# Kernel optimization log

Hardware: AMD Instinct MI355X
Metric: run time of the kernel (lower is better)

Reference implementation:

```python
import jax, jax.numpy as jnp
from jax import lax
import numpy as np

THRESHOLD = 0.9
KHALF = 5  # conv_kernel_size; full conv width = 2*KHALF + 1 = 11


def _cif_scan(eouts, alpha_norm, elens, ylens, Lp1):
    """Vectorized-over-batch integrate-and-fire scan over time (lax.scan)."""
    B, T, D = eouts.shape
    bidx = jnp.arange(B)
    dt = eouts.dtype

    def step(carry, xs):
        alpha_accum, state, n_tok, fired = carry
        a_t, e_t, t = xs  # a_t: [B], e_t: [B,D], t: scalar int
        alpha_accum = alpha_accum + a_t
        active = (t <= elens - 1) & (n_tok < ylens)
        fire = active & (alpha_accum >= THRESHOLD)
        ak1 = 1.0 - alpha_accum
        ak2 = a_t - ak1
        # attention-weight column for time t
        aw_col = jnp.zeros((B, Lp1), dt)
        w_old = jnp.where(fire, ak1, jnp.where(active, a_t, jnp.zeros((), dt)))
        aw_col = aw_col.at[bidx, n_tok].add(w_old)
        n_new = n_tok + fire.astype(n_tok.dtype)
        aw_col = aw_col.at[bidx, n_new].add(jnp.where(fire, ak2, jnp.zeros((), dt)))
        # fired output row (set once per token slot)
        fire_val = state + ak1[:, None] * e_t
        cur = fired[bidx, n_tok]
        fired = fired.at[bidx, n_tok].set(jnp.where(fire[:, None], fire_val, cur))
        # integrate / reset state
        state = jnp.where(fire[:, None], ak2[:, None] * e_t,
                          jnp.where(active[:, None], state + a_t[:, None] * e_t, state))
        alpha_accum = jnp.where(fire, ak2, alpha_accum)
        return (alpha_accum, state, n_new, fired), aw_col

    init = (jnp.zeros((B,), dt), jnp.zeros((B, D), dt),
            jnp.zeros((B,), jnp.int32), jnp.zeros((B, Lp1, D), dt))
    xs = (jnp.swapaxes(alpha_norm, 0, 1), jnp.swapaxes(eouts, 0, 1),
          jnp.arange(T))
    (_, _, _, fired), aw_cols = lax.scan(step, init, xs)
    aws = jnp.transpose(aw_cols, (1, 2, 0))[:, None]  # [B,1,Lp1,T]
    return fired, aws


def _forward(eouts, conv_w, conv_b, proj_w, proj_b, elens, ylens, L):
    # Conv1d over time, 'same' padding: [B,T,D] -> [B,T,C]
    conv_feat = lax.conv_general_dilated(
        eouts, conv_w, window_strides=(1,), padding=[(KHALF, KHALF)],
        dimension_numbers=('NWC', 'WIO', 'NWC')) + conv_b
    alpha = jax.nn.sigmoid(conv_feat @ proj_w + proj_b)[:, :, 0]  # [B,T]
    alpha_norm = alpha / jnp.sum(alpha, axis=1, keepdims=True) \
        * ylens[:, None].astype(alpha.dtype)
    fired, aws = _cif_scan(eouts, alpha_norm, elens, ylens, L + 1)
    return fired[:, :L], alpha, aws


def setup_inputs():
    key = jax.random.key(0)
    k1, k2, k3, k4, k5 = jax.random.split(key, 5)
    B, T, D, C = 16, 2048, 512, 512
    eouts = jax.random.normal(k1, (B, T, D), jnp.float32)
    elens = jnp.maximum(jax.random.randint(k2, (B,), 0, T), T // 2).astype(jnp.int32)
    ylens = jnp.maximum(jax.random.randint(k3, (B,), 0, 128), 32).astype(jnp.int32)
    conv_w = jax.random.normal(k4, (2 * KHALF + 1, D, C), jnp.float32) * 0.02
    conv_b = jnp.zeros((C,), jnp.float32)
    proj_w = jax.random.normal(k5, (C, 1), jnp.float32) * 0.05
    proj_b = jnp.zeros((1,), jnp.float32)
    return dict(eouts=eouts, conv_w=conv_w, conv_b=conv_b,
                proj_w=proj_w, proj_b=proj_b, elens=elens, ylens=ylens)


def reference(eouts, conv_w, conv_b, proj_w, proj_b, elens, ylens):
    L = int(jnp.max(ylens))  # max_len = ylens.max(), as in the original
    return _forward(eouts, conv_w, conv_b, proj_w, proj_b, elens, ylens, L)
```

## Files before the change

kernel.cpp:

```cpp
#include <hip/hip_runtime.h>
#include <math.h>

#define KHALF 5
#define MAXF 256

__device__ inline float readlane_f(float v, int lane) {
    return __int_as_float(__builtin_amdgcn_readlane(__float_as_int(v), lane));
}

__global__ void k_prep(const float* __restrict__ conv_w, const float* __restrict__ conv_b,
                       const float* __restrict__ proj_w, const float* __restrict__ proj_b,
                       float* __restrict__ w_eff, float* __restrict__ b_eff,
                       int KD, int C,
                       float* __restrict__ aws, long long awsN, int WB, int NFILL) {
    if ((int)blockIdx.x >= WB) {
        long long N4 = awsN >> 2;
        long long gid = (long long)(blockIdx.x - WB) * 256 + threadIdx.x;
        float4 z = make_float4(0.f, 0.f, 0.f, 0.f);
        float4* a4 = reinterpret_cast<float4*>(aws);
        long long stride = (long long)NFILL * 256;
        for (long long i = gid; i < N4; i += stride) a4[i] = z;
        int tail = (int)(awsN & 3);
        if (gid < tail) aws[4 * N4 + gid] = 0.f;
        return;
    }
    int gid = blockIdx.x * blockDim.x + threadIdx.x;
    int wave = gid >> 6;
    int lane = gid & 63;
    if (wave > KD) return;
    float s = 0.f;
    if (wave < KD) {
        const float* row = conv_w + (size_t)wave * C;
        for (int c = lane * 4; c < C; c += 256) {
            float4 v = *reinterpret_cast<const float4*>(row + c);
            float4 w = *reinterpret_cast<const float4*>(proj_w + c);
            s += v.x * w.x + v.y * w.y + v.z * w.z + v.w * w.w;
        }
    } else {
        for (int c = lane; c < C; c += 64) s += conv_b[c] * proj_w[c];
    }
#pragma unroll
    for (int off = 32; off > 0; off >>= 1) s += __shfl_down(s, off, 64);
    if (lane == 0) {
        if (wave < KD) w_eff[wave] = s;
        else           b_eff[0] = s + proj_b[0];
    }
}

__global__ __launch_bounds__(256) void k_qdot(const float* __restrict__ eouts,
                                              const float* __restrict__ w_eff,
                                              float* __restrict__ q, int BT) {
    __shared__ float tile[64 * 68];
    __shared__ float wls[11 * 68];
    __shared__ float part[64 * 89];
    const int u0 = blockIdx.x * 64;
    const int rp = threadIdx.x & 31;
    const int s8 = threadIdx.x >> 5;
    float acc0[11], acc1[11];
#pragma unroll
    for (int k = 0; k < 11; ++k) { acc0[k] = 0.f; acc1[k] = 0.f; }
    for (int c = 0; c < 8; ++c) {
        __syncthreads();
#pragma unroll
        for (int it = 0; it < 4; ++it) {
            int idx = it * 256 + threadIdx.x;
            int r = idx >> 4, j4 = idx & 15;
            float4 v = *reinterpret_cast<const float4*>(
                eouts + (size_t)(u0 + r) * 512 + c * 64 + j4 * 4);
            *reinterpret_cast<float4*>(&tile[r * 68 + j4 * 4]) = v;
        }
        if (threadIdx.x < 176) {
            int k = threadIdx.x >> 4, sl = threadIdx.x & 15;
            float4 wv = *reinterpret_cast<const float4*>(
                w_eff + k * 512 + c * 64 + sl * 4);
            *reinterpret_cast<float4*>(&wls[k * 68 + sl * 4]) = wv;
        }
        __syncthreads();
#pragma unroll
        for (int j4 = 0; j4 < 2; ++j4) {
            const int dl = s8 * 8 + j4 * 4;
            float4 a0 = *reinterpret_cast<const float4*>(&tile[rp * 68 + dl]);
            float4 a1 = *reinterpret_cast<const float4*>(&tile[(rp + 32) * 68 + dl]);
#pragma unroll
            for (int k = 0; k < 11; ++k) {
                float4 wv = *reinterpret_cast<const float4*>(&wls[k * 68 + dl]);
                acc0[k] += a0.x * wv.x + a0.y * wv.y + a0.z * wv.z + a0.w * wv.w;
                acc1[k] += a1.x * wv.x + a1.y * wv.y + a1.z * wv.z + a1.w * wv.w;
            }
        }
    }
    __syncthreads();
#pragma unroll
    for (int k = 0; k < 11; ++k) {
        part[rp * 89 + s8 * 11 + k] = acc0[k];
        part[(rp + 32) * 89 + s8 * 11 + k] = acc1[k];
    }
    __syncthreads();
    if (threadIdx.x < 64) {
        int r = threadIdx.x;
        const float* p = &part[r * 89];
        float o[12];
#pragma unroll
        for (int k = 0; k < 11; ++k) {
            float s0 = (p[0 * 11 + k] + p[1 * 11 + k]) + (p[2 * 11 + k] + p[3 * 11 + k]);
            float s1 = (p[4 * 11 + k] + p[5 * 11 + k]) + (p[6 * 11 + k] + p[7 * 11 + k]);
            o[k] = s0 + s1;
        }
        o[11] = 0.f;
        float4* dst = reinterpret_cast<float4*>(q + (size_t)(u0 + r) * 12);
        dst[0] = make_float4(o[0], o[1], o[2], o[3]);
        dst[1] = make_float4(o[4], o[5], o[6], o[7]);
        dst[2] = make_float4(o[8], o[9], o[10], o[11]);
    }
}

__global__ __launch_bounds__(256) void k_sigpart(const float* __restrict__ q,
                                                 const float* __restrict__ b_eff,
                                                 float* __restrict__ alpha,
                                                 float* __restrict__ partials,
                                                 int T, int tcb) {
    __shared__ float qs[266 * 12];
    __shared__ float psm[4];
    int bx = blockIdx.x;
    int b = bx / tcb, tc = bx % tcb;
    int t0 = tc * 256;
    const float* qb = q + (size_t)b * T * 12;
    const int base = (t0 - 5) * 12;
    const int lim = T * 12;
    for (int i = threadIdx.x; i < 266 * 12; i += 256) {
        int gi = base + i;
        qs[i] = (gi >= 0 && gi < lim) ? qb[gi] : 0.f;
    }
    __syncthreads();
    int t = t0 + threadIdx.x;
    float sacc = b_eff[0];
#pragma unroll
    for (int k = 0; k < 11; ++k) sacc += qs[(threadIdx.x + k) * 12 + k];
    float al = 1.f / (1.f + expf(-sacc));
    alpha[(size_t)b * T + t] = al;
    float s = al;
    int lane = threadIdx.x & 63;
    int w = threadIdx.x >> 6;
#pragma unroll
    for (int off = 32; off > 0; off >>= 1) s += __shfl_down(s, off, 64);
    if (lane == 0) psm[w] = s;
    __syncthreads();
    if (threadIdx.x == 0) {
        float tot = 0.f;
        for (int i = 0; i < 4; ++i) tot += psm[i];
        partials[bx] = tot;
    }
}

__global__ void k_alpha(const float* __restrict__ eouts,
                        const float* __restrict__ w_eff,
                        const float* __restrict__ b_eff,
                        float* __restrict__ alpha,
                        int B, int T, int D) {
    const int W = 2 * KHALF + 1;
    int gid = blockIdx.x * blockDim.x + threadIdx.x;
    int wave = gid >> 6;
    int lane = gid & 63;
    if (wave >= B * T) return;
    int b = wave / T;
    int t = wave - b * T;
    int WD = W * D;
    int t0 = t - KHALF;
    float s = 0.f;
    if (t0 >= 0 && t0 + W <= T) {
        const float* base = eouts + ((size_t)b * T + t0) * D;
        for (int j = lane * 4; j < WD; j += 256) {
            float4 v = *reinterpret_cast<const float4*>(base + j);
            float4 w = *reinterpret_cast<const float4*>(w_eff + j);
            s += v.x * w.x + v.y * w.y + v.z * w.z + v.w * w.w;
        }
    } else {
        const float* base = eouts + (size_t)b * T * D;
        for (int j = lane; j < WD; j += 64) {
            int tt = t0 + j / D;
            if (tt >= 0 && tt < T) {
                int d = j - (j / D) * D;
                s += base[(size_t)tt * D + d] * w_eff[j];
            }
        }
    }
#pragma unroll
    for (int off = 32; off > 0; off >>= 1) s += __shfl_down(s, off, 64);
    if (lane == 0) {
        float logit = s + b_eff[0];
        alpha[(size_t)b * T + t] = 1.f / (1.f + expf(-logit));
    }
}

__global__ void k_chain(const float* __restrict__ alpha_in,
                        int use_part,
                        const float* __restrict__ partials, int npart,
                        const int* __restrict__ elens,
                        const int* __restrict__ ylens,
                        float* __restrict__ anorm,
                        int* __restrict__ n_fired,
                        int* __restrict__ fire_t,
                        float* __restrict__ fire_a1,
                        float* __restrict__ fire_a2,
                        int T, int Lp1) {
    extern __shared__ float an[];
    float* pf = an + T;
    __shared__ float sm[16];
    __shared__ float stot;
    int b = blockIdx.x;
    const float* row = alpha_in + (size_t)b * T;
    if ((T & 1023) == 0) {
        const float4* r4 = reinterpret_cast<const float4*>(row);
        float4* a4 = reinterpret_cast<float4*>(an);
        for (int i = threadIdx.x; i < (T >> 2); i += blockDim.x) a4[i] = r4[i];
    } else {
        for (int i = threadIdx.x; i < T; i += blockDim.x) an[i] = row[i];
    }
    __syncthreads();
    if (use_part) {
        if (threadIdx.x < npart && threadIdx.x < 16)
            sm[threadIdx.x] = partials[b * npart + threadIdx.x];
        __syncthreads();
        if (threadIdx.x == 0) {
            float tot = 0.f;
            if (npart <= 16) { for (int i = 0; i < npart; ++i) tot += sm[i]; }
            else { for (int i = 0; i < npart; ++i) tot += partials[b * npart + i]; }
            stot = tot;
        }
    } else {
        float s = 0.f;
        for (int i = threadIdx.x; i < T; i += blockDim.x) s += an[i];
        int lane0 = threadIdx.x & 63;
        int w0 = threadIdx.x >> 6;
#pragma unroll
        for (int off = 32; off > 0; off >>= 1) s += __shfl_down(s, off, 64);
        if (lane0 == 0) sm[w0] = s;
        __syncthreads();
        if (threadIdx.x == 0) {
            float tot = 0.f;
            int nw = blockDim.x >> 6;
            for (int i = 0; i < nw; ++i) tot += sm[i];
            stot = tot;
        }
    }
    __syncthreads();
    float ssum = stot;
    float yl = (float)ylens[b];
    float* __restrict__ anb = anorm + (size_t)b * T;
    for (int i = threadIdx.x; i < T; i += blockDim.x) {
        float v = an[i] / ssum * yl;
        an[i] = v;
        anb[i] = v;
    }
    __syncthreads();
    {
        int wv = threadIdx.x >> 6, ln = threadIdx.x & 63;
        int nchunks = (T + 63) >> 6;
        for (int c = wv; c < nchunks; c += 4) {
            int t = c * 64 + ln;
            float P = (t < T) ? an[t] : 0.f;
#pragma unroll
            for (int off = 1; off < 64; off <<= 1) {
                float tmp = __shfl_up(P, off, 64);
                if (ln >= off) P += tmp;
            }
            if (t < T) pf[t] = P;
        }
    }
    __syncthreads();
    if (threadIdx.x >= 64) return;
    int lane = threadIdx.x;
    int elen = elens[b];
    if (elen > T) elen = T;
    const int ylen = ylens[b];
    int* __restrict__ ft = fire_t + (size_t)b * Lp1;
    float* __restrict__ fa1 = fire_a1 + (size_t)b * Lp1;
    float* __restrict__ fa2 = fire_a2 + (size_t)b * Lp1;
    float accum = 0.f;
    int n = 0;
    bool done = false;
    for (int t0 = 0; t0 < elen && !done; t0 += 64) {
        int nv = elen - t0;
        if (nv > 64) nv = 64;
        bool inb = (t0 + lane < T);
        float P = inb ? pf[t0 + lane] : 0.f;
        float av = inb ? an[t0 + lane] : 0.f;
        unsigned long long validmask = (nv == 64) ? ~0ull : ((1ull << nv) - 1ull);
        float base = accum;
        int start = 0;
        while (true) {
            bool cond = (base + P >= 0.9f);
            unsigned long long bal = __ballot(cond) & validmask;
            if (start > 0) bal &= (~0ull) << start;
            if (bal == 0) break;
            int u = __builtin_ctzll(bal);
            float Pu = readlane_f(P, u);
            float au = readlane_f(av, u);
            float accum_f = base + Pu;
            float ak1 = 1.f - accum_f;
            float ak2 = au - ak1;
            if (lane == 0) { ft[n] = t0 + u; fa1[n] = ak1; fa2[n] = ak2; }
            ++n;
            if (n >= ylen) { done = true; break; }
            base = ak2 - Pu;
            start = u + 1;
            if (start >= nv) break;
        }
        if (!done) accum = base + readlane_f(P, nv - 1);
    }
    if (lane == 0) n_fired[b] = n;
}

__global__ void k_awfired(const float* __restrict__ eouts,
                          const float* __restrict__ anorm,
                          const int* __restrict__ elens,
                          const int* __restrict__ ylens,
                          const int* __restrict__ n_fired,
                          const int* __restrict__ fire_t,
                          const float* __restrict__ fire_a1,
                          const float* __restrict__ fire_a2,
                          float* __restrict__ aws,
                          float* __restrict__ fired,
                          int T, int D, int L, int Lp1,
                          int AB, int tcpb) {
    if ((int)blockIdx.x < AB) {
        __shared__ int fts[MAXF];
        __shared__ float a1s[MAXF];
        __shared__ float a2s[MAXF];
        int b = blockIdx.x / tcpb;
        int tc = blockIdx.x % tcpb;
        int nf = n_fired[b];
        for (int i = threadIdx.x; i < nf; i += blockDim.x) {
            fts[i] = fire_t[(size_t)b * Lp1 + i];
            a1s[i] = fire_a1[(size_t)b * Lp1 + i];
            a2s[i] = fire_a2[(size_t)b * Lp1 + i];
        }
        __syncthreads();
        int t = tc * 256 + threadIdx.x;
        if (t >= T) return;
        int elen = elens[b];
        if (elen > T) elen = T;
        int ylen = ylens[b];
        if (t >= elen) return;
        int lo = 0, hi = nf;
        while (lo < hi) {
            int mid = (lo + hi) >> 1;
            if (fts[mid] < t) lo = mid + 1; else hi = mid;
        }
        int rowi = lo;
        bool isfire = (rowi < nf && fts[rowi] == t);
        float* col = aws + (size_t)b * Lp1 * T + t;
        if (isfire) {
            col[(size_t)rowi * T] = a1s[rowi];
            col[(size_t)(rowi + 1) * T] = a2s[rowi];
        } else if (rowi < ylen) {
            col[(size_t)rowi * T] = anorm[(size_t)b * T + t];
        }
    } else {
        __shared__ float4 red[128];
        int idx = blockIdx.x - AB;
        int b = idx / L;
        int n = idx % L;
        int h = threadIdx.x >> 7;
        int dl = threadIdx.x & 127;
        int nf = n_fired[b];
        if ((D & 3) == 0) {
            int D4 = D >> 2;
            float4* dst = reinterpret_cast<float4*>(fired + ((size_t)b * L + n) * D);
            if (n >= nf) {
                if (h == 0) {
                    for (int d4 = dl; d4 < D4; d4 += 128)
                        dst[d4] = make_float4(0.f, 0.f, 0.f, 0.f);
                }
                return;
            }
            int t0 = (n == 0) ? 0 : fire_t[(size_t)b * Lp1 + n - 1];
            int t1 = fire_t[(size_t)b * Lp1 + n];
            float ak1 = fire_a1[(size_t)b * Lp1 + n];
            float ak2p = (n > 0) ? fire_a2[(size_t)b * Lp1 + n - 1] : 0.f;
            const float* an_g = anorm + (size_t)b * T;
            float wfirst = (n > 0) ? ak2p : an_g[t0];
            int len = t1 - t0 + 1;
            int half0 = len >> 1;
            int ts = h ? (t0 + half0) : t0;
            int te = h ? t1 : (t0 + half0 - 1);
            const float4* Eb = reinterpret_cast<const float4*>(eouts + (size_t)b * T * D);
            for (int d0 = 0; d0 < D4; d0 += 128) {
                int d4 = d0 + dl;
                float4 acc = make_float4(0.f, 0.f, 0.f, 0.f);
                if (d4 < D4 && ts <= te) {
                    float4 a0 = acc, a1 = acc, a2 = acc, a3 = acc;
                    int t = ts;
                    const float4* ee = Eb + (size_t)ts * D4 + d4;
                    for (; t + 3 <= te; t += 4, ee += 4 * (size_t)D4) {
                        float w0 = (t == t1)     ? ak1 : ((t == t0)     ? wfirst : an_g[t]);
                        float w1 = (t + 1 == t1) ? ak1 : an_g[t + 1];
                        float w2 = (t + 2 == t1) ? ak1 : an_g[t + 2];
                        float w3 = (t + 3 == t1) ? ak1 : an_g[t + 3];
                        float4 va = ee[0], vb = ee[D4], vc = ee[2 * (size_t)D4], vd = ee[3 * (size_t)D4];
                        a0.x += w0 * va.x; a0.y += w0 * va.y; a0.z += w0 * va.z; a0.w += w0 * va.w;
                        a1.x += w1 * vb.x; a1.y += w1 * vb.y; a1.z += w1 * vb.z; a1.w += w1 * vb.w;
                        a2.x += w2 * vc.x; a2.y += w2 * vc.y; a2.z += w2 * vc.z; a2.w += w2 * vc.w;
                        a3.x += w3 * vd.x; a3.y += w3 * vd.y; a3.z += w3 * vd.z; a3.w += w3 * vd.w;
                    }
                    for (; t <= te; ++t, ee += D4) {
                        float wt = (t == t1) ? ak1 : ((t == t0) ? wfirst : an_g[t]);
                        float4 v = ee[0];
                        a0.x += wt * v.x; a0.y += wt * v.y; a0.z += wt * v.z; a0.w += wt * v.w;
                    }
                    acc.x = (a0.x + a1.x) + (a2.x + a3.x);
                    acc.y = (a0.y + a1.y) + (a2.y + a3.y);
                    acc.z = (a0.z + a1.z) + (a2.z + a3.z);
                    acc.w = (a0.w + a1.w) + (a2.w + a3.w);
                }
                if (h == 1 && d4 < D4) red[dl] = acc;
                __syncthreads();
                if (h == 0 && d4 < D4) {
                    float4 o = red[dl];
                    acc.x += o.x; acc.y += o.y; acc.z += o.z; acc.w += o.w;
                    dst[d4] = acc;
                }
                __syncthreads();
            }
        } else {
            float* dst = fired + ((size_t)b * L + n) * D;
            if (n >= nf) {
                for (int d = threadIdx.x; d < D; d += 256) dst[d] = 0.f;
                return;
            }
            int t0 = (n == 0) ? 0 : fire_t[(size_t)b * Lp1 + n - 1];
            int t1 = fire_t[(size_t)b * Lp1 + n];
            float ak1 = fire_a1[(size_t)b * Lp1 + n];
            float ak2p = (n > 0) ? fire_a2[(size_t)b * Lp1 + n - 1] : 0.f;
            const float* an_g = anorm + (size_t)b * T;
            for (int d = threadIdx.x; d < D; d += 256) {
                const float* e = eouts + ((size_t)b * T + t0) * D + d;
                float accv;
                if (t1 == t0) {
                    accv = ak1 * e[0];
                } else {
                    float w0 = (n > 0) ? ak2p : an_g[t0];
                    accv = w0 * e[0];
                    float a0 = 0.f, a1 = 0.f, a2 = 0.f, a3 = 0.f;
                    int t = t0 + 1;
                    const float* ee = e + D;
                    for (; t + 3 < t1; t += 4, ee += 4 * (size_t)D) {
                        a0 += an_g[t]     * ee[0];
                        a1 += an_g[t + 1] * ee[D];
                        a2 += an_g[t + 2] * ee[2 * (size_t)D];
                        a3 += an_g[t + 3] * ee[3 * (size_t)D];
                    }
                    for (; t < t1; ++t, ee += D) a0 += an_g[t] * ee[0];
                    accv += ((a0 + a1) + (a2 + a3));
                    accv += ak1 * ee[0];
                }
                dst[d] = accv;
            }
        }
    }
}

extern "C" void kernel_launch(void* const* d_in, const int* in_sizes, int n_in,
                              void* d_out, int out_size, void* d_ws, size_t ws_size,
                              hipStream_t stream) {
    const float* eouts  = (const float*)d_in[0];
    const float* conv_w = (const float*)d_in[1];
    const float* conv_b = (const float*)d_in[2];
    const float* proj_w = (const float*)d_in[3];
    const float* proj_b = (const float*)d_in[4];
    const int*   elens  = (const int*)d_in[5];
    const int*   ylens  = (const int*)d_in[6];

    const int B = in_sizes[5];
    const int C = in_sizes[2];
    const int W = 2 * KHALF + 1;
    const int D = in_sizes[1] / (W * C);
    const int T = in_sizes[0] / (B * D);
    const int L = (out_size - 2 * B * T) / (B * (D + T));
    const int Lp1 = L + 1;
    const int BT = B * T;
    const int tcb = (T + 255) / 256;

    float* out   = (float*)d_out;
    float* fired = out;
    float* alpha = out + (size_t)B * L * D;
    float* aws   = alpha + (size_t)B * T;

    char*  ws        = (char*)d_ws;
    float* w_eff     = (float*)ws;
    float* b_eff     = (float*)(ws + (size_t)W * D * 4);
    int*   n_fired   = (int*)(b_eff + 16);
    int*   fire_t    = n_fired + B + 16;
    float* fire_a1   = (float*)(fire_t + (size_t)B * Lp1 + 16);
    float* fire_a2   = fire_a1 + (size_t)B * Lp1 + 16;
    float* anorm     = fire_a2 + (size_t)B * Lp1 + 16;
    float* qbuf      = anorm + (size_t)B * T + 16;
    float* partials  = qbuf + (size_t)BT * 12 + 16;
    size_t ws_need   = (size_t)((char*)(partials + (size_t)B * tcb + 16) - ws);

    const int KD = W * D;
    {
        long long wthreads = (long long)(KD + 1) * 64;
        int WB = (int)((wthreads + 255) / 256);
        int NFILL = 2048;
        long long awsN = (long long)B * Lp1 * T;
        k_prep<<<WB + NFILL, 256, 0, stream>>>(conv_w, conv_b, proj_w, proj_b,
                                               w_eff, b_eff, KD, C,
                                               aws, awsN, WB, NFILL);
    }

    const bool fast = (ws_size >= ws_need) && (D == 512) && (C == 512) &&
                      (BT % 64 == 0) && (T % 256 == 0) && (T <= 16384) &&
                      (Lp1 <= MAXF);
    if (fast) {
        k_qdot<<<BT / 64, 256, 0, stream>>>(eouts, w_eff, qbuf, BT);
        k_sigpart<<<B * tcb, 256, 0, stream>>>(qbuf, b_eff, alpha, partials, T, tcb);
    } else {
        long long threads = (long long)BT * 64;
        int blocks = (int)((threads + 255) / 256);
        k_alpha<<<blocks, 256, 0, stream>>>(eouts, w_eff, b_eff, alpha, B, T, D);
    }

    k_chain<<<B, 256, 2 * T * sizeof(float), stream>>>(
        alpha, fast ? 1 : 0, partials, tcb,
        elens, ylens, anorm,
        n_fired, fire_t, fire_a1, fire_a2, T, Lp1);

    {
        int tcpb = (T + 255) / 256;
        int AB = B * tcpb;
        int FB = B * L;
        k_awfired<<<AB + FB, 256, 0, stream>>>(eouts, anorm,
                                               elens, ylens, n_fired,
                                               fire_t, fire_a1, fire_a2,
                                               aws, fired, T, D, L, Lp1,
                                               AB, tcpb);
    }
}
```

Measured before the change: 160.8 us.

## Fuse sigmoid partial-sum and chain kernels with atomic-counter cross-block handoff

Merges the sigmoid/partial-sum kernel and the per-batch fire-chain kernel into one launch. Producer blocks publish their partial sums and bump a per-batch counter, and B trailing consumer blocks spin until all partials for their row are in before running the normalisation, prefix scan and fire search. This removes one kernel launch and the serialisation gap between the two stages. In exchange it relies on the trailing blocks being scheduled after the producers, guarded by limits on B and grid size, and it adds spin-wait and atomic traffic.

```diff
diff --git a/kernel.cpp b/kernel.cpp
--- a/kernel.cpp
+++ b/kernel.cpp
@@ -11,6 +11,7 @@
 __global__ void k_prep(const float* __restrict__ conv_w, const float* __restrict__ conv_b,
                        const float* __restrict__ proj_w, const float* __restrict__ proj_b,
                        float* __restrict__ w_eff, float* __restrict__ b_eff,
+                       int* __restrict__ counters, int B,
                        int KD, int C,
                        float* __restrict__ aws, long long awsN, int WB, int NFILL) {
     if ((int)blockIdx.x >= WB) {
@@ -37,6 +38,7 @@
             s += v.x * w.x + v.y * w.y + v.z * w.z + v.w * w.w;
         }
     } else {
+        if (lane >= 1 && lane <= B) counters[lane - 1] = 0;
         for (int c = lane; c < C; c += 64) s += conv_b[c] * proj_w[c];
     }
 #pragma unroll
@@ -114,42 +116,156 @@
     }
 }
 
-__global__ __launch_bounds__(256) void k_sigpart(const float* __restrict__ q,
-                                                 const float* __restrict__ b_eff,
-                                                 float* __restrict__ alpha,
-                                                 float* __restrict__ partials,
-                                                 int T, int tcb) {
+__global__ __launch_bounds__(256) void k_sigchain(
+        const float* __restrict__ q,
+        const float* __restrict__ b_eff,
+        float* __restrict__ alpha,
+        float* __restrict__ partials,
+        int* __restrict__ counters,
+        const int* __restrict__ elens,
+        const int* __restrict__ ylens,
+        float* __restrict__ anorm,
+        int* __restrict__ n_fired,
+        int* __restrict__ fire_t,
+        float* __restrict__ fire_a1,
+        float* __restrict__ fire_a2,
+        int T, int Lp1, int tcb, int SB) {
+    extern __shared__ float an[];
     __shared__ float qs[266 * 12];
     __shared__ float psm[4];
+    __shared__ float sm[16];
+    __shared__ float stot;
     int bx = blockIdx.x;
-    int b = bx / tcb, tc = bx % tcb;
-    int t0 = tc * 256;
-    const float* qb = q + (size_t)b * T * 12;
-    const int base = (t0 - 5) * 12;
-    const int lim = T * 12;
-    for (int i = threadIdx.x; i < 266 * 12; i += 256) {
-        int gi = base + i;
-        qs[i] = (gi >= 0 && gi < lim) ? qb[gi] : 0.f;
-    }
-    __syncthreads();
-    int t = t0 + threadIdx.x;
-    float sacc = b_eff[0];
-#pragma unroll
-    for (int k = 0; k < 11; ++k) sacc += qs[(threadIdx.x + k) * 12 + k];
-    float al = 1.f / (1.f + expf(-sacc));
-    alpha[(size_t)b * T + t] = al;
-    float s = al;
-    int lane = threadIdx.x & 63;
-    int w = threadIdx.x >> 6;
-#pragma unroll
-    for (int off = 32; off > 0; off >>= 1) s += __shfl_down(s, off, 64);
-    if (lane == 0) psm[w] = s;
+
+    if (bx < SB) {
+        int b = bx / tcb, tc = bx % tcb;
+        int t0 = tc * 256;
+        const float* qb = q + (size_t)b * T * 12;
+        const int base = (t0 - 5) * 12;
+        const int lim = T * 12;
+        for (int i = threadIdx.x; i < 266 * 12; i += 256) {
+            int gi = base + i;
+            qs[i] = (gi >= 0 && gi < lim) ? qb[gi] : 0.f;
+        }
+        __syncthreads();
+        int t = t0 + threadIdx.x;
+        float sacc = b_eff[0];
+#pragma unroll
+        for (int k = 0; k < 11; ++k) sacc += qs[(threadIdx.x + k) * 12 + k];
+        float al = 1.f / (1.f + expf(-sacc));
+        alpha[(size_t)b * T + t] = al;
+        float s = al;
+        int lane = threadIdx.x & 63;
+        int w = threadIdx.x >> 6;
+#pragma unroll
+        for (int off = 32; off > 0; off >>= 1) s += __shfl_down(s, off, 64);
+        if (lane == 0) psm[w] = s;
+        __syncthreads();
+        if (threadIdx.x == 0) {
+            float tot = 0.f;
+            for (int i = 0; i < 4; ++i) tot += psm[i];
+            partials[bx] = tot;
+            __threadfence();
+            atomicAdd(&counters[b], 1);
+        }
+        return;
+    }
+
+    int b = bx - SB;
+    if (threadIdx.x == 0) {
+        while (atomicAdd(&counters[b], 0) < tcb) {
+            __builtin_amdgcn_s_sleep(2);
+        }
+    }
+    __syncthreads();
+    __threadfence();
+
+    const float* row = alpha + (size_t)b * T;
+    if ((T & 1023) == 0) {
+        const float4* r4 = reinterpret_cast<const float4*>(row);
+        float4* a4 = reinterpret_cast<float4*>(an);
+        for (int i = threadIdx.x; i < (T >> 2); i += blockDim.x) a4[i] = r4[i];
+    } else {
+        for (int i = threadIdx.x; i < T; i += blockDim.x) an[i] = row[i];
+    }
+    __syncthreads();
+    if (threadIdx.x < tcb && threadIdx.x < 16)
+        sm[threadIdx.x] = partials[b * tcb + threadIdx.x];
     __syncthreads();
     if (threadIdx.x == 0) {
         float tot = 0.f;
-        for (int i = 0; i < 4; ++i) tot += psm[i];
-        partials[bx] = tot;
-    }
+        if (tcb <= 16) { for (int i = 0; i < tcb; ++i) tot += sm[i]; }
+        else { for (int i = 0; i < tcb; ++i) tot += partials[b * tcb + i]; }
+        stot = tot;
+    }
+    __syncthreads();
+    float ssum = stot;
+    float yl = (float)ylens[b];
+    float* __restrict__ anb = anorm + (size_t)b * T;
+    for (int i = threadIdx.x; i < T; i += blockDim.x) {
+        float v = an[i] / ssum * yl;
+        an[i] = v;
+        anb[i] = v;
+    }
+    __syncthreads();
+    {
+        float* pf = an + T;
+        int wv = threadIdx.x >> 6, ln = threadIdx.x & 63;
+        int nchunks = (T + 63) >> 6;
+        for (int c = wv; c < nchunks; c += 4) {
+            int t = c * 64 + ln;
+            float P = (t < T) ? an[t] : 0.f;
+#pragma unroll
+            for (int off = 1; off < 64; off <<= 1) {
+                float tmp = __shfl_up(P, off, 64);
+                if (ln >= off) P += tmp;
+            }
+            if (t < T) pf[t] = P;
+        }
+    }
+    __syncthreads();
+    if (threadIdx.x >= 64) return;
+    float* pf = an + T;
+    int lane = threadIdx.x;
+    int elen = elens[b];
+    if (elen > T) elen = T;
+    const int ylen = ylens[b];
+    int* __restrict__ ft = fire_t + (size_t)b * Lp1;
+    float* __restrict__ fa1 = fire_a1 + (size_t)b * Lp1;
+    float* __restrict__ fa2 = fire_a2 + (size_t)b * Lp1;
+    float accum = 0.f;
+    int n = 0;
+    bool done = false;
+    for (int t0 = 0; t0 < elen && !done; t0 += 64) {
+        int nv = elen - t0;
+        if (nv > 64) nv = 64;
+        bool inb = (t0 + lane < T);
+        float P = inb ? pf[t0 + lane] : 0.f;
+        float av = inb ? an[t0 + lane] : 0.f;
+        unsigned long long validmask = (nv == 64) ? ~0ull : ((1ull << nv) - 1ull);
+        float base = accum;
+        int start = 0;
+        while (true) {
+            bool cond = (base + P >= 0.9f);
+            unsigned long long bal = __ballot(cond) & validmask;
+            if (start > 0) bal &= (~0ull) << start;
+            if (bal == 0) break;
+            int u = __builtin_ctzll(bal);
+            float Pu = readlane_f(P, u);
+            float au = readlane_f(av, u);
+            float accum_f = base + Pu;
+            float ak1 = 1.f - accum_f;
+            float ak2 = au - ak1;
+            if (lane == 0) { ft[n] = t0 + u; fa1[n] = ak1; fa2[n] = ak2; }
+            ++n;
+            if (n >= ylen) { done = true; break; }
+            base = ak2 - Pu;
+            start = u + 1;
+            if (start >= nv) break;
+        }
+        if (!done) accum = base + readlane_f(P, nv - 1);
+    }
+    if (lane == 0) n_fired[b] = n;
 }
 
 __global__ void k_alpha(const float* __restrict__ eouts,
@@ -193,8 +309,6 @@
 }
 
 __global__ void k_chain(const float* __restrict__ alpha_in,
-                        int use_part,
-                        const float* __restrict__ partials, int npart,
                         const int* __restrict__ elens,
                         const int* __restrict__ ylens,
                         float* __restrict__ anorm,
@@ -209,25 +323,9 @@
     __shared__ float stot;
     int b = blockIdx.x;
     const float* row = alpha_in + (size_t)b * T;
-    if ((T & 1023) == 0) {
-        const float4* r4 = reinterpret_cast<const float4*>(row);
-        float4* a4 = reinterpret_cast<float4*>(an);
-        for (int i = threadIdx.x; i < (T >> 2); i += blockDim.x) a4[i] = r4[i];
-    } else {
-        for (int i = threadIdx.x; i < T; i += blockDim.x) an[i] = row[i];
-    }
-    __syncthreads();
-    if (use_part) {
-        if (threadIdx.x < npart && threadIdx.x < 16)
-            sm[threadIdx.x] = partials[b * npart + threadIdx.x];
-        __syncthreads();
-        if (threadIdx.x == 0) {
-            float tot = 0.f;
-            if (npart <= 16) { for (int i = 0; i < npart; ++i) tot += sm[i]; }
-            else { for (int i = 0; i < npart; ++i) tot += partials[b * npart + i]; }
-            stot = tot;
-        }
-    } else {
+    for (int i = threadIdx.x; i < T; i += blockDim.x) an[i] = row[i];
+    __syncthreads();
+    {
         float s = 0.f;
         for (int i = threadIdx.x; i < T; i += blockDim.x) s += an[i];
         int lane0 = threadIdx.x & 63;
@@ -496,7 +594,8 @@
     float* anorm     = fire_a2 + (size_t)B * Lp1 + 16;
     float* qbuf      = anorm + (size_t)B * T + 16;
     float* partials  = qbuf + (size_t)BT * 12 + 16;
-    size_t ws_need   = (size_t)((char*)(partials + (size_t)B * tcb + 16) - ws);
+    int*   counters  = (int*)(partials + (size_t)B * tcb + 16);
+    size_t ws_need   = (size_t)((char*)(counters + B + 16) - ws);
 
     const int KD = W * D;
     {
@@ -505,26 +604,28 @@
         int NFILL = 2048;
         long long awsN = (long long)B * Lp1 * T;
         k_prep<<<WB + NFILL, 256, 0, stream>>>(conv_w, conv_b, proj_w, proj_b,
-                                               w_eff, b_eff, KD, C,
+                                               w_eff, b_eff, counters, B, KD, C,
                                                aws, awsN, WB, NFILL);
     }
 
     const bool fast = (ws_size >= ws_need) && (D == 512) && (C == 512) &&
                       (BT % 64 == 0) && (T % 256 == 0) && (T <= 16384) &&
-                      (Lp1 <= MAXF);
+                      (Lp1 <= MAXF) && (B <= 63) && (B * tcb + B <= 4096);
     if (fast) {
         k_qdot<<<BT / 64, 256, 0, stream>>>(eouts, w_eff, qbuf, BT);
-        k_sigpart<<<B * tcb, 256, 0, stream>>>(qbuf, b_eff, alpha, partials, T, tcb);
+        int SB = B * tcb;
+        k_sigchain<<<SB + B, 256, 2 * T * sizeof(float), stream>>>(
+            qbuf, b_eff, alpha, partials, counters,
+            elens, ylens, anorm,
+            n_fired, fire_t, fire_a1, fire_a2, T, Lp1, tcb, SB);
     } else {
         long long threads = (long long)BT * 64;
         int blocks = (int)((threads + 255) / 256);
         k_alpha<<<blocks, 256, 0, stream>>>(eouts, w_eff, b_eff, alpha, B, T, D);
-    }
-
-    k_chain<<<B, 256, 2 * T * sizeof(float), stream>>>(
-        alpha, fast ? 1 : 0, partials, tcb,
-        elens, ylens, anorm,
-        n_fired, fire_t, fire_a1, fire_a2, T, Lp1);
+        k_chain<<<B, 256, 2 * T * sizeof(float), stream>>>(
+            alpha, elens, ylens, anorm,
+            n_fired, fire_t, fire_a1, fire_a2, T, Lp1);
+    }
 
     {
         int tcpb = (T + 255) / 256;
```

After: 166.4 us. 1.04x slower.
